# Performance work log

Measured on AMD Instinct MI355X. Metric: run time of the kernel, lower is better.

## Reference

```python
import jax, jax.numpy as jnp
import numpy as np

B, N, D, L = 8, 2048, 1024, 128


def setup_inputs() -> dict:
    key = jax.random.key(0)
    ks = jax.random.split(key, 8)
    return {
        "e_i_t_minus_1": jax.random.normal(ks[0], (B, D), dtype=jnp.float32),
        "e_j_t": jax.random.normal(ks[1], (B, N, D), dtype=jnp.float32),
        "imp_j_t": jax.random.uniform(ks[2], (B, N), dtype=jnp.float32),
        "R_lk": jax.random.normal(ks[3], (L, D), dtype=jnp.float32),
        "W_q": jax.random.normal(ks[4], (D, D), dtype=jnp.float32) * (D ** -0.5),
        "W_k": jax.random.normal(ks[5], (D, D), dtype=jnp.float32) * (D ** -0.5),
        "W_v": jax.random.normal(ks[6], (D, D), dtype=jnp.float32) * (D ** -0.5),
        "omega": jax.random.normal(ks[7], (D,), dtype=jnp.float32),
    }


def reference(e_i_t_minus_1, e_j_t, imp_j_t, R_lk, W_q, W_k, W_v, omega):
    # torch nn.Linear(x) = x @ W.T  (weights stored [out, in])
    q_i = jnp.einsum('bd,ed->be', e_i_t_minus_1, W_q)[:, None, :]   # [B,1,D]
    k_j = jnp.einsum('bnd,ed->bne', e_j_t, W_k)                      # [B,N,D]
    sigma = jnp.einsum('bnd,d->bn', jnp.tanh(q_i + k_j), omega)      # [B,N]
    exp_sigma = jnp.exp(sigma)
    sum_exp = jnp.sum(exp_sigma, axis=1, keepdims=True)              # [B,1]
    a_ij = imp_j_t * exp_sigma / (sum_exp + 1e-9)                    # [B,N]
    v_j = jnp.einsum('bnd,ed->bne', e_j_t, W_v)                      # [B,N,D]
    A = jnp.einsum('bn,bnd->bd', a_ij, v_j)                          # [B,D]
    # R_lk[l,d] * a_ij[b,n] * v_j[b,n,d], summed over n -> [B,L,D]
    A_lk = jnp.einsum('bn,bnd,ld->bld', a_ij, v_j, R_lk)             # [B,L,D]
    A_l = A                                                          # identical math in source
    return (A, A_lk, A_l)
```

## Files before the change

kernel.cpp:

```cpp
#include <hip/hip_runtime.h>
#include <hip/hip_bf16.h>
#include <math.h>

#define BB 8
#define NN 2048
#define DD 1024
#define LL 128
#define MM (BB*NN)

typedef _Float16 half8 __attribute__((ext_vector_type(8)));
typedef _Float16 half4 __attribute__((ext_vector_type(4)));
typedef __attribute__((ext_vector_type(4))) float floatx4;

__device__ __forceinline__ void glds16(const void* g, void* l) {
    __builtin_amdgcn_global_load_lds(
        (const __attribute__((address_space(1))) unsigned int*)g,
        (__attribute__((address_space(3))) unsigned int*)l, 16, 0, 0);
}

__global__ __launch_bounds__(256) void prep_kernel(const float* __restrict__ e_j,
                                                   _Float16* __restrict__ eh,
                                                   const float* __restrict__ Wk,
                                                   _Float16* __restrict__ wh,
                                                   const float* __restrict__ e_i,
                                                   const float* __restrict__ Wq,
                                                   float* __restrict__ q) {
    __shared__ float us[BB][DD];
    int blk = blockIdx.x;
    int tid = threadIdx.x;
    if (blk < 8192) {
        int i = blk * 256 + tid;
        const float4* xp = (const float4*)e_j + (size_t)i * 2;
        float4 v0 = xp[0], v1 = xp[1];
        half8 h;
        h[0] = (_Float16)v0.x; h[1] = (_Float16)v0.y;
        h[2] = (_Float16)v0.z; h[3] = (_Float16)v0.w;
        h[4] = (_Float16)v1.x; h[5] = (_Float16)v1.y;
        h[6] = (_Float16)v1.z; h[7] = (_Float16)v1.w;
        *(half8*)(eh + (size_t)i * 8) = h;
    } else if (blk < 8704) {
        int i = (blk - 8192) * 256 + tid;
        const float4* xp = (const float4*)Wk + (size_t)i * 2;
        float4 v0 = xp[0], v1 = xp[1];
        half8 h;
        h[0] = (_Float16)v0.x; h[1] = (_Float16)v0.y;
        h[2] = (_Float16)v0.z; h[3] = (_Float16)v0.w;
        h[4] = (_Float16)v1.x; h[5] = (_Float16)v1.y;
        h[6] = (_Float16)v1.z; h[7] = (_Float16)v1.w;
        *(half8*)(wh + (size_t)i * 8) = h;
    } else {
        for (int i = tid; i < BB * DD / 4; i += 256)
            ((float4*)&us[0][0])[i] = ((const float4*)e_i)[i];
        __syncthreads();
        int w = tid >> 6, lane = tid & 63;
        int d = (blk - 8704) * 4 + w;
        float acc[8] = {0.f, 0.f, 0.f, 0.f, 0.f, 0.f, 0.f, 0.f};
        for (int e0 = 0; e0 < DD; e0 += 256) {
            float4 wv = *(const float4*)&Wq[(size_t)d * DD + e0 + lane * 4];
            #pragma unroll
            for (int r = 0; r < 8; ++r) {
                float4 uv = *(const float4*)&us[r][e0 + lane * 4];
                acc[r] += wv.x * uv.x + wv.y * uv.y + wv.z * uv.z + wv.w * uv.w;
            }
        }
        #pragma unroll
        for (int r = 0; r < 8; ++r) {
            float s = acc[r];
            #pragma unroll
            for (int off = 32; off; off >>= 1) s += __shfl_down(s, off, 64);
            if (lane == 0) q[r * DD + d] = s;
        }
    }
}

__global__ __launch_bounds__(256) void sigma_mfma(const _Float16* __restrict__ eh,
                                                  const _Float16* __restrict__ wh,
                                                  const float* __restrict__ q,
                                                  const float* __restrict__ omega,
                                                  float* __restrict__ sig_part)
{
    __shared__ _Float16 Ah[128][32];
    __shared__ _Float16 Bh[128][32];
    __shared__ float red[128][2];

    const int tid  = threadIdx.x;
    const int lane = tid & 63;
    const int w    = tid >> 6;
    const int wr   = w >> 1, wc = w & 1;
    const int c15  = lane & 15, quad = lane >> 4;

    const int row0 = blockIdx.x * 128;
    const int col0 = blockIdx.y * 128;
    const int b    = row0 / NN;

    const int r0 = tid >> 2;
    const int ku = (tid & 3) * 8;

    const _Float16* gA = eh + (size_t)(row0 + r0) * DD + ku;
    const _Float16* gB = wh + (size_t)(col0 + r0) * DD + ku;

    char* dA = (char*)&Ah[0][0] + w * 1024;
    char* dB = (char*)&Bh[0][0] + w * 1024;

    floatx4 acc[4][4];
    #pragma unroll
    for (int i = 0; i < 4; ++i)
        #pragma unroll
        for (int j = 0; j < 4; ++j)
            acc[i][j] = (floatx4){0.f, 0.f, 0.f, 0.f};

    for (int k0 = 0; k0 < DD; k0 += 32) {
        glds16(gA + k0,                   dA);
        glds16(gA + (size_t)64 * DD + k0, dA + 4096);
        glds16(gB + k0,                   dB);
        glds16(gB + (size_t)64 * DD + k0, dB + 4096);
        __syncthreads();

        half8 a[4], bf[4];
        #pragma unroll
        for (int i = 0; i < 4; ++i) {
            a[i]  = *(const half8*)&Ah[wr * 64 + i * 16 + c15][quad * 8];
            bf[i] = *(const half8*)&Bh[wc * 64 + i * 16 + c15][quad * 8];
        }
        #pragma unroll
        for (int i = 0; i < 4; ++i)
            #pragma unroll
            for (int j = 0; j < 4; ++j)
                acc[i][j] = __builtin_amdgcn_mfma_f32_16x16x32_f16(a[i], bf[j], acc[i][j], 0, 0, 0);
        __syncthreads();
    }

    float part[4][4];
    #pragma unroll
    for (int i = 0; i < 4; ++i)
        #pragma unroll
        for (int r = 0; r < 4; ++r) part[i][r] = 0.f;

    #pragma unroll
    for (int j = 0; j < 4; ++j) {
        int c = col0 + wc * 64 + j * 16 + c15;
        float qv = q[b * DD + c];
        float om = omega[c];
        #pragma unroll
        for (int i = 0; i < 4; ++i)
            #pragma unroll
            for (int r = 0; r < 4; ++r)
                part[i][r] += tanhf(acc[i][j][r] + qv) * om;
    }
    #pragma unroll
    for (int i = 0; i < 4; ++i)
        #pragma unroll
        for (int r = 0; r < 4; ++r) {
            float s = part[i][r];
            s += __shfl_xor(s, 1, 64);
            s += __shfl_xor(s, 2, 64);
            s += __shfl_xor(s, 4, 64);
            s += __shfl_xor(s, 8, 64);
            if (c15 == 0) red[wr * 64 + i * 16 + quad * 4 + r][wc] = s;
        }
    __syncthreads();
    if (tid < 128)
        sig_part[blockIdx.y * MM + row0 + tid] = red[tid][0] + red[tid][1];
}

__global__ __launch_bounds__(256) void softmax_k(const float* __restrict__ sig_part,
                                                 const float* __restrict__ imp,
                                                 float* __restrict__ a_ij) {
    int b = blockIdx.x >> 3, slice = blockIdx.x & 7;
    int tid = threadIdx.x;
    __shared__ float red[256];
    float sv[8];
    float m = -1e30f;
    #pragma unroll
    for (int p = 0; p < 8; ++p) {
        int n = p * 256 + tid;
        float s = 0.f;
        #pragma unroll
        for (int db = 0; db < 8; ++db) s += sig_part[db * MM + b * NN + n];
        sv[p] = s;
        m = fmaxf(m, s);
    }
    red[tid] = m; __syncthreads();
    for (int off = 128; off; off >>= 1) {
        if (tid < off) red[tid] = fmaxf(red[tid], red[tid + off]);
        __syncthreads();
    }
    m = red[0]; __syncthreads();
    float sum = 0.f;
    #pragma unroll
    for (int p = 0; p < 8; ++p) sum += expf(sv[p] - m);
    red[tid] = sum; __syncthreads();
    for (int off = 128; off; off >>= 1) {
        if (tid < off) red[tid] += red[tid + off];
        __syncthreads();
    }
    float inv = 1.f / (red[0] + 1e-9f * expf(-m));
    int n = slice * 256 + tid;
    a_ij[b * NN + n] = imp[b * NN + n] * expf(sv[slice] - m) * inv;
}

__global__ __launch_bounds__(256) void u_kernel(const float* __restrict__ a_ij,
                                                const _Float16* __restrict__ eh,
                                                float* __restrict__ u_part) {
    int b = blockIdx.x >> 7, nc = blockIdx.x & 127;
    int t = threadIdx.x;
    float4 acc = {0.f, 0.f, 0.f, 0.f};
    const _Float16* base = eh + ((size_t)(b * NN + nc * 16)) * DD + t * 4;
    const float* ap = a_ij + b * NN + nc * 16;
    #pragma unroll
    for (int n = 0; n < 16; ++n) {
        float a = ap[n];
        half4 v = *(const half4*)(base + (size_t)n * DD);
        acc.x += a * (float)v[0]; acc.y += a * (float)v[1];
        acc.z += a * (float)v[2]; acc.w += a * (float)v[3];
    }
    *(float4*)(u_part + ((size_t)nc * BB + b) * DD + t * 4) = acc;
}

__global__ __launch_bounds__(256) void ureduce(const float* __restrict__ u_part,
                                               float* __restrict__ u) {
    int i = blockIdx.x * 256 + threadIdx.x;
    float s = 0.f;
    #pragma unroll 8
    for (int nc = 0; nc < 128; ++nc) s += u_part[(size_t)nc * BB * DD + i];
    u[i] = s;
}

__global__ __launch_bounds__(256) void rowdot8(const float* __restrict__ X,
                                               const float* __restrict__ W,
                                               float* __restrict__ out) {
    __shared__ float us[BB][DD];
    int tid = threadIdx.x;
    for (int i = tid; i < BB * DD / 4; i += 256)
        ((float4*)&us[0][0])[i] = ((const float4*)X)[i];
    __syncthreads();
    int w = tid >> 6, lane = tid & 63;
    int d = blockIdx.x * 4 + w;
    float acc[8] = {0.f, 0.f, 0.f, 0.f, 0.f, 0.f, 0.f, 0.f};
    for (int e0 = 0; e0 < DD; e0 += 256) {
        float4 wv = *(const float4*)&W[(size_t)d * DD + e0 + lane * 4];
        #pragma unroll
        for (int r = 0; r < 8; ++r) {
            float4 uv = *(const float4*)&us[r][e0 + lane * 4];
            acc[r] += wv.x * uv.x + wv.y * uv.y + wv.z * uv.z + wv.w * uv.w;
        }
    }
    #pragma unroll
    for (int r = 0; r < 8; ++r) {
        float s = acc[r];
        #pragma unroll
        for (int off = 32; off; off >>= 1) s += __shfl_down(s, off, 64);
        if (lane == 0) out[r * DD + d] = s;
    }
}

__global__ __launch_bounds__(256) void out_kernel(const float* __restrict__ A,
                                                  const float* __restrict__ Rlk,
                                                  float* __restrict__ out) {
    int i = blockIdx.x * 256 + threadIdx.x;
    int d = i & (DD - 1);
    int l = (i >> 10) & (LL - 1);
    int b = i >> 17;
    out[BB * DD + i] = A[b * DD + d] * Rlk[l * DD + d];
    if (i < BB * DD) {
        out[i] = A[i];
        out[BB * DD + BB * LL * DD + i] = A[i];
    }
}

extern "C" void kernel_launch(void* const* d_in, const int* in_sizes, int n_in,
                              void* d_out, int out_size, void* d_ws, size_t ws_size,
                              hipStream_t stream) {
    const float* e_i   = (const float*)d_in[0];
    const float* e_j   = (const float*)d_in[1];
    const float* imp   = (const float*)d_in[2];
    const float* Rlk   = (const float*)d_in[3];
    const float* Wq    = (const float*)d_in[4];
    const float* Wk    = (const float*)d_in[5];
    const float* Wv    = (const float*)d_in[6];
    const float* omega = (const float*)d_in[7];
    float* out = (float*)d_out;
    float* ws  = (float*)d_ws;

    float* q    = ws;
    float* sigp = ws + 8192;
    float* a_ij = ws + 139264;
    float* u    = ws + 155648;
    _Float16* eh = (_Float16*)(ws + 172032);
    _Float16* wh = eh + (size_t)MM * DD;
    float* u_part = (float*)(wh + (size_t)DD * DD);

    prep_kernel<<<8960, 256, 0, stream>>>(e_j, eh, Wk, wh, e_i, Wq, q);

    sigma_mfma<<<dim3(MM / 128, DD / 128), 256, 0, stream>>>(eh, wh, q, omega, sigp);

    softmax_k<<<64, 256, 0, stream>>>(sigp, imp, a_ij);

    u_kernel<<<1024, 256, 0, stream>>>(a_ij, eh, u_part);
    ureduce<<<32, 256, 0, stream>>>(u_part, u);

    rowdot8<<<256, 256, 0, stream>>>(u, Wv, a_ij);

    out_kernel<<<(BB * LL * DD) / 256, 256, 0, stream>>>(a_ij, Rlk, out);
}
```

Measured before the change: 209.7 us.

## Double-buffer sigma GEMM LDS tiles and split prep kernel into three launches

The sigma MFMA GEMM now uses two LDS buffers for its A and B tiles. It prefetches the next K-slice with global_load_lds while computing on the current one, which drops one barrier per iteration and overlaps global loads with MFMA work. The combined prep kernel is split into separate e_j conversion, W_k conversion and q-projection kernels. This stops the 32 KB shared array from being reserved by every conversion block, at the cost of two extra launches. Double-buffering doubles the GEMM's LDS footprint and relies on the barrier waiting for outstanding LDS-direct loads.

```diff
diff --git a/kernel.cpp b/kernel.cpp
--- a/kernel.cpp
+++ b/kernel.cpp
@@ -18,58 +18,57 @@
         (__attribute__((address_space(3))) unsigned int*)l, 16, 0, 0);
 }
 
-__global__ __launch_bounds__(256) void prep_kernel(const float* __restrict__ e_j,
-                                                   _Float16* __restrict__ eh,
-                                                   const float* __restrict__ Wk,
-                                                   _Float16* __restrict__ wh,
-                                                   const float* __restrict__ e_i,
-                                                   const float* __restrict__ Wq,
-                                                   float* __restrict__ q) {
+__global__ __launch_bounds__(256) void prep_ej(const float* __restrict__ e_j,
+                                               _Float16* __restrict__ eh) {
+    int i = blockIdx.x * 256 + threadIdx.x;
+    const float4* xp = (const float4*)e_j + (size_t)i * 2;
+    float4 v0 = xp[0], v1 = xp[1];
+    half8 h;
+    h[0] = (_Float16)v0.x; h[1] = (_Float16)v0.y;
+    h[2] = (_Float16)v0.z; h[3] = (_Float16)v0.w;
+    h[4] = (_Float16)v1.x; h[5] = (_Float16)v1.y;
+    h[6] = (_Float16)v1.z; h[7] = (_Float16)v1.w;
+    *(half8*)(eh + (size_t)i * 8) = h;
+}
+
+__global__ __launch_bounds__(256) void prep_wk(const float* __restrict__ Wk,
+                                               _Float16* __restrict__ wh) {
+    int i = blockIdx.x * 256 + threadIdx.x;
+    const float4* xp = (const float4*)Wk + (size_t)i * 2;
+    float4 v0 = xp[0], v1 = xp[1];
+    half8 h;
+    h[0] = (_Float16)v0.x; h[1] = (_Float16)v0.y;
+    h[2] = (_Float16)v0.z; h[3] = (_Float16)v0.w;
+    h[4] = (_Float16)v1.x; h[5] = (_Float16)v1.y;
+    h[6] = (_Float16)v1.z; h[7] = (_Float16)v1.w;
+    *(half8*)(wh + (size_t)i * 8) = h;
+}
+
+__global__ __launch_bounds__(256) void prep_q(const float* __restrict__ e_i,
+                                              const float* __restrict__ Wq,
+                                              float* __restrict__ q) {
     __shared__ float us[BB][DD];
-    int blk = blockIdx.x;
     int tid = threadIdx.x;
-    if (blk < 8192) {
-        int i = blk * 256 + tid;
-        const float4* xp = (const float4*)e_j + (size_t)i * 2;
-        float4 v0 = xp[0], v1 = xp[1];
-        half8 h;
-        h[0] = (_Float16)v0.x; h[1] = (_Float16)v0.y;
-        h[2] = (_Float16)v0.z; h[3] = (_Float16)v0.w;
-        h[4] = (_Float16)v1.x; h[5] = (_Float16)v1.y;
-        h[6] = (_Float16)v1.z; h[7] = (_Float16)v1.w;
-        *(half8*)(eh + (size_t)i * 8) = h;
-    } else if (blk < 8704) {
-        int i = (blk - 8192) * 256 + tid;
-        const float4* xp = (const float4*)Wk + (size_t)i * 2;
-        float4 v0 = xp[0], v1 = xp[1];
-        half8 h;
-        h[0] = (_Float16)v0.x; h[1] = (_Float16)v0.y;
-        h[2] = (_Float16)v0.z; h[3] = (_Float16)v0.w;
-        h[4] = (_Float16)v1.x; h[5] = (_Float16)v1.y;
-        h[6] = (_Float16)v1.z; h[7] = (_Float16)v1.w;
-        *(half8*)(wh + (size_t)i * 8) = h;
-    } else {
-        for (int i = tid; i < BB * DD / 4; i += 256)
-            ((float4*)&us[0][0])[i] = ((const float4*)e_i)[i];
-        __syncthreads();
-        int w = tid >> 6, lane = tid & 63;
-        int d = (blk - 8704) * 4 + w;
-        float acc[8] = {0.f, 0.f, 0.f, 0.f, 0.f, 0.f, 0.f, 0.f};
-        for (int e0 = 0; e0 < DD; e0 += 256) {
-            float4 wv = *(const float4*)&Wq[(size_t)d * DD + e0 + lane * 4];
-            #pragma unroll
-            for (int r = 0; r < 8; ++r) {
-                float4 uv = *(const float4*)&us[r][e0 + lane * 4];
-                acc[r] += wv.x * uv.x + wv.y * uv.y + wv.z * uv.z + wv.w * uv.w;
-            }
-        }
+    for (int i = tid; i < BB * DD / 4; i += 256)
+        ((float4*)&us[0][0])[i] = ((const float4*)e_i)[i];
+    __syncthreads();
+    int w = tid >> 6, lane = tid & 63;
+    int d = blockIdx.x * 4 + w;
+    float acc[8] = {0.f, 0.f, 0.f, 0.f, 0.f, 0.f, 0.f, 0.f};
+    for (int e0 = 0; e0 < DD; e0 += 256) {
+        float4 wv = *(const float4*)&Wq[(size_t)d * DD + e0 + lane * 4];
         #pragma unroll
         for (int r = 0; r < 8; ++r) {
-            float s = acc[r];
-            #pragma unroll
-            for (int off = 32; off; off >>= 1) s += __shfl_down(s, off, 64);
-            if (lane == 0) q[r * DD + d] = s;
-        }
+            float4 uv = *(const float4*)&us[r][e0 + lane * 4];
+            acc[r] += wv.x * uv.x + wv.y * uv.y + wv.z * uv.z + wv.w * uv.w;
+        }
+    }
+    #pragma unroll
+    for (int r = 0; r < 8; ++r) {
+        float s = acc[r];
+        #pragma unroll
+        for (int off = 32; off; off >>= 1) s += __shfl_down(s, off, 64);
+        if (lane == 0) q[r * DD + d] = s;
     }
 }
 
@@ -79,8 +78,8 @@
                                                   const float* __restrict__ omega,
                                                   float* __restrict__ sig_part)
 {
-    __shared__ _Float16 Ah[128][32];
-    __shared__ _Float16 Bh[128][32];
+    __shared__ _Float16 Ah[2][128][32];
+    __shared__ _Float16 Bh[2][128][32];
     __shared__ float red[128][2];
 
     const int tid  = threadIdx.x;
@@ -99,8 +98,8 @@
     const _Float16* gA = eh + (size_t)(row0 + r0) * DD + ku;
     const _Float16* gB = wh + (size_t)(col0 + r0) * DD + ku;
 
-    char* dA = (char*)&Ah[0][0] + w * 1024;
-    char* dB = (char*)&Bh[0][0] + w * 1024;
+    char* dA[2] = { (char*)&Ah[0][0][0] + w * 1024, (char*)&Ah[1][0][0] + w * 1024 };
+    char* dB[2] = { (char*)&Bh[0][0][0] + w * 1024, (char*)&Bh[1][0][0] + w * 1024 };
 
     floatx4 acc[4][4];
     #pragma unroll
@@ -109,25 +108,33 @@
         for (int j = 0; j < 4; ++j)
             acc[i][j] = (floatx4){0.f, 0.f, 0.f, 0.f};
 
+    glds16(gA,                   dA[0]);
+    glds16(gA + (size_t)64 * DD, dA[0] + 4096);
+    glds16(gB,                   dB[0]);
+    glds16(gB + (size_t)64 * DD, dB[0] + 4096);
+
     for (int k0 = 0; k0 < DD; k0 += 32) {
-        glds16(gA + k0,                   dA);
-        glds16(gA + (size_t)64 * DD + k0, dA + 4096);
-        glds16(gB + k0,                   dB);
-        glds16(gB + (size_t)64 * DD + k0, dB + 4096);
+        const int s = (k0 >> 5) & 1;
         __syncthreads();
+        if (k0 + 32 < DD) {
+            const int n = s ^ 1;
+            glds16(gA + k0 + 32,                   dA[n]);
+            glds16(gA + (size_t)64 * DD + k0 + 32, dA[n] + 4096);
+            glds16(gB + k0 + 32,                   dB[n]);
+            glds16(gB + (size_t)64 * DD + k0 + 32, dB[n] + 4096);
+        }
 
         half8 a[4], bf[4];
         #pragma unroll
         for (int i = 0; i < 4; ++i) {
-            a[i]  = *(const half8*)&Ah[wr * 64 + i * 16 + c15][quad * 8];
-            bf[i] = *(const half8*)&Bh[wc * 64 + i * 16 + c15][quad * 8];
+            a[i]  = *(const half8*)&Ah[s][wr * 64 + i * 16 + c15][quad * 8];
+            bf[i] = *(const half8*)&Bh[s][wc * 64 + i * 16 + c15][quad * 8];
         }
         #pragma unroll
         for (int i = 0; i < 4; ++i)
             #pragma unroll
             for (int j = 0; j < 4; ++j)
                 acc[i][j] = __builtin_amdgcn_mfma_f32_16x16x32_f16(a[i], bf[j], acc[i][j], 0, 0, 0);
-        __syncthreads();
     }
 
     float part[4][4];
@@ -290,7 +297,9 @@
     _Float16* wh = eh + (size_t)MM * DD;
     float* u_part = (float*)(wh + (size_t)DD * DD);
 
-    prep_kernel<<<8960, 256, 0, stream>>>(e_j, eh, Wk, wh, e_i, Wq, q);
+    prep_ej<<<8192, 256, 0, stream>>>(e_j, eh);
+    prep_wk<<<512, 256, 0, stream>>>(Wk, wh);
+    prep_q<<<256, 256, 0, stream>>>(e_i, Wq, q);
 
     sigma_mfma<<<dim3(MM / 128, DD / 128), 256, 0, stream>>>(eh, wh, q, omega, sigp);
 
```

Result: slower. 221.4 us (+5.6%).
